# Kernel optimization log

Hardware: AMD Instinct MI355X
Metric: run time of the kernel (lower is better)

Reference implementation:

```python
import jax, jax.numpy as jnp
import numpy as np

NUM_EXPERTS = 8
TOP_K = 2
ENTROPY_WEIGHT = 0.1
MAX_USAGE_RATIO = 0.3


def setup_inputs() -> dict:
    key = jax.random.key(0)
    k0, k1, k2 = jax.random.split(key, 3)
    B, S, D, H, E = 4, 4096, 1024, 1024, NUM_EXPERTS
    x = jax.random.normal(k0, (B, S, D), jnp.float32)
    gate_w = jax.random.normal(k1, (D, E), jnp.float32) * (1.0 / np.sqrt(D))
    gate_b = jnp.zeros((E,), jnp.float32)
    expert_w = jax.random.normal(k2, (E, D, H), jnp.float32) * (1.0 / np.sqrt(D))
    expert_b = jnp.zeros((E, H), jnp.float32)
    return {"x": x, "gate_w": gate_w, "gate_b": gate_b,
            "expert_w": expert_w, "expert_b": expert_b}


def reference(x, gate_w, gate_b, expert_w, expert_b):
    # x: [B, S, D]; dropout omitted (eval mode / deterministic reference)
    B, S, D = x.shape
    E = gate_w.shape[1]
    H = expert_w.shape[2]
    N = B * S
    xf = x.reshape(N, D)

    gate_logits = xf @ gate_w + gate_b            # [N, E]
    gate_probs = jax.nn.softmax(gate_logits, axis=-1)
    entropy = -jnp.sum(gate_probs * jnp.log(gate_probs + 1e-10), axis=-1).mean()
    entropy_loss = ENTROPY_WEIGHT * entropy

    topk_probs, topk_idx = jax.lax.top_k(gate_probs, TOP_K)   # [N, K]
    onehot = jax.nn.one_hot(topk_idx, E, dtype=xf.dtype)       # [N, K, E]
    combine = jnp.einsum('nk,nke->ne', topk_probs, onehot)     # [N, E] gating weight per expert

    # Weighted combine of per-expert Linear outputs; loop over small fixed E.
    out = jnp.zeros((N, H), xf.dtype)
    for e in range(E):
        out = out + combine[:, e:e + 1] * (xf @ expert_w[e] + expert_b[e])

    counts = jnp.sum(onehot, axis=(0, 1))                      # [E] tokens routed per expert
    usage_ratios = counts / N
    overuse_penalty = jnp.sum(jax.nn.relu(usage_ratios - MAX_USAGE_RATIO))

    return out.reshape(B, S, H), entropy_loss + overuse_penalty
```

## Files before the change

### kernel.cpp

```cpp
#include <hip/hip_runtime.h>
#include <hip/hip_bf16.h>

typedef __bf16 bf16x8 __attribute__((ext_vector_type(8)));
typedef __bf16 bf16x4 __attribute__((ext_vector_type(4)));
typedef float  f32x4  __attribute__((ext_vector_type(4)));

#define NTOK 16384
#define DDIM 1024
#define HDIM 1024
#define NEXP 8

#define XB_OFF   0u
#define WT_OFF   33554432u
#define IDX_OFF  50331648u
#define PRB_OFF  50855936u
#define TTE_OFF  51380224u
#define TTP_OFF  51511296u
#define CNT_OFF  51642368u
#define ENT_OFF  51642400u

typedef __attribute__((address_space(1))) void gvoid_t;
typedef __attribute__((address_space(3))) void lvoid_t;

__device__ __forceinline__ void cp16(void* lds, const void* g) {
  __builtin_amdgcn_global_load_lds((gvoid_t*)g, (lvoid_t*)lds, 16, 0, 0);
}

__global__ __launch_bounds__(256) void transpose_w(const float* __restrict__ w,
                                                   __bf16* __restrict__ wT) {
  const int e  = blockIdx.z;
  const int d0 = blockIdx.y * 64;
  const int h0 = blockIdx.x * 64;
  __shared__ float tile[64][68];
  const int t = threadIdx.x;
  const float* base = w + ((size_t)e * DDIM + d0) * HDIM + h0;
#pragma unroll
  for (int it = 0; it < 4; ++it) {
    int dl = it * 16 + (t >> 4);
    int hl = (t & 15) * 4;
    float4 v = *(const float4*)(base + (size_t)dl * HDIM + hl);
    tile[dl][hl]     = v.x;
    tile[dl][hl + 1] = v.y;
    tile[dl][hl + 2] = v.z;
    tile[dl][hl + 3] = v.w;
  }
  __syncthreads();
  __bf16* obase = wT + ((size_t)e * HDIM + h0) * DDIM + d0;
#pragma unroll
  for (int it = 0; it < 4; ++it) {
    int hl = it * 16 + (t >> 4);
    int dl = (t & 15) * 4;
    bf16x4 bv;
    bv[0] = (__bf16)tile[dl][hl];
    bv[1] = (__bf16)tile[dl + 1][hl];
    bv[2] = (__bf16)tile[dl + 2][hl];
    bv[3] = (__bf16)tile[dl + 3][hl];
    *(bf16x4*)(obase + (size_t)hl * DDIM + dl) = bv;
  }
}

__global__ __launch_bounds__(256) void gate_kernel(
    const float* __restrict__ x, const float* __restrict__ gw,
    const float* __restrict__ gb, __bf16* __restrict__ xb,
    int* __restrict__ idx_g, float* __restrict__ prob_g,
    int2* __restrict__ tt_e, float2* __restrict__ tt_p,
    int* __restrict__ cnt_g, float* __restrict__ ent_g) {
  __shared__ float gwT[8 * 1040];
  __shared__ int   lidx[8 * 64];
  __shared__ float lprob[8 * 64];
  __shared__ int   lcnt[8];
  __shared__ int   gbase[8];
  __shared__ float went[4];
  const int tid = threadIdx.x, w = tid >> 6, lane = tid & 63;
  if (tid < 8) lcnt[tid] = 0;
#pragma unroll
  for (int i = 0; i < 32; ++i) {
    int lin = i * 256 + tid;
    gwT[(lin & 7) * 1040 + (lin >> 3)] = gw[lin];
  }
  __syncthreads();

  float entacc = 0.f;
  for (int t = 0; t < 8; ++t) {
    const int n = blockIdx.x * 32 + w * 8 + t;
    const float4* xr = (const float4*)(x + (size_t)n * DDIM);
    float acc[8] = {0.f, 0.f, 0.f, 0.f, 0.f, 0.f, 0.f, 0.f};
#pragma unroll
    for (int i = 0; i < 4; ++i) {
      float4 v = xr[i * 64 + lane];
      bf16x4 bv;
      bv[0] = (__bf16)v.x; bv[1] = (__bf16)v.y;
      bv[2] = (__bf16)v.z; bv[3] = (__bf16)v.w;
      *(bf16x4*)(xb + (size_t)n * DDIM + i * 256 + lane * 4) = bv;
#pragma unroll
      for (int e = 0; e < 8; ++e) {
        float4 g = *(const float4*)&gwT[e * 1040 + i * 256 + lane * 4];
        acc[e] += v.x * g.x + v.y * g.y + v.z * g.z + v.w * g.w;
      }
    }
#pragma unroll
    for (int e = 0; e < 8; ++e) {
      float s = acc[e];
      for (int off = 32; off; off >>= 1) s += __shfl_down(s, off);
      acc[e] = s;
    }
    if (lane == 0) {
      float p[8];
      float mx = -1e30f;
#pragma unroll
      for (int e = 0; e < 8; ++e) { p[e] = acc[e] + gb[e]; mx = fmaxf(mx, p[e]); }
      float s = 0.f;
#pragma unroll
      for (int e = 0; e < 8; ++e) { p[e] = expf(p[e] - mx); s += p[e]; }
      float inv = 1.0f / s;
      float ent = 0.f;
#pragma unroll
      for (int e = 0; e < 8; ++e) { p[e] *= inv; ent -= p[e] * logf(p[e] + 1e-10f); }
      entacc += ent;
      int e1 = 0; float p1 = p[0];
#pragma unroll
      for (int e = 1; e < 8; ++e) if (p[e] > p1) { p1 = p[e]; e1 = e; }
      int e2 = (e1 == 0) ? 1 : 0; float p2 = p[e2];
#pragma unroll
      for (int e = 0; e < 8; ++e) if (e != e1 && p[e] > p2) { p2 = p[e]; e2 = e; }
      tt_e[n] = make_int2(e1, e2);
      tt_p[n] = make_float2(p1, p2);
      int j = atomicAdd(&lcnt[e1], 1); lidx[e1 * 64 + j] = n; lprob[e1 * 64 + j] = p1;
      j = atomicAdd(&lcnt[e2], 1);     lidx[e2 * 64 + j] = n; lprob[e2 * 64 + j] = p2;
    }
  }
  if (lane == 0) went[w] = entacc;
  __syncthreads();
  if (tid < 8) gbase[tid] = atomicAdd(&cnt_g[tid], lcnt[tid]);
  if (tid == 0) atomicAdd(ent_g, went[0] + went[1] + went[2] + went[3]);
  __syncthreads();
#pragma unroll
  for (int e = 0; e < 8; ++e) {
    for (int j = tid; j < lcnt[e]; j += 256) {
      idx_g[e * NTOK + gbase[e] + j]  = lidx[e * 64 + j];
      prob_g[e * NTOK + gbase[e] + j] = lprob[e * 64 + j];
    }
  }
}

__global__ __launch_bounds__(256) void init_out(const int2* __restrict__ tt_e,
                                                const float2* __restrict__ tt_p,
                                                const float* __restrict__ eb,
                                                float* __restrict__ out) {
  const int n = blockIdx.x, t = threadIdx.x;
  int2   ee = tt_e[n];
  float2 pp = tt_p[n];
  float4 v1 = ((const float4*)(eb + (size_t)ee.x * HDIM))[t];
  float4 v2 = ((const float4*)(eb + (size_t)ee.y * HDIM))[t];
  float4 r;
  r.x = pp.x * v1.x + pp.y * v2.x;
  r.y = pp.x * v1.y + pp.y * v2.y;
  r.z = pp.x * v1.z + pp.y * v2.z;
  r.w = pp.x * v1.w + pp.y * v2.w;
  ((float4*)(out + (size_t)n * HDIM))[t] = r;
}

__global__ __launch_bounds__(256) void moe_gemm(
    const __bf16* __restrict__ xb, const __bf16* __restrict__ wT,
    const int* __restrict__ idx_g, const float* __restrict__ prob_g,
    const int* __restrict__ cnt_g, float* __restrict__ out) {
  const int e = blockIdx.z, gy = blockIdx.y, gx = blockIdx.x;
  const int cnt = cnt_g[e];
  if (gy * 128 >= cnt) return;

  __shared__ __bf16 Ash[128 * 64];
  __shared__ __bf16 Bsh[128 * 64];
  __shared__ int    tok_s[128];
  __shared__ float  p_s[128];

  const int tid = threadIdx.x, w = tid >> 6, lane = tid & 63;
  if (tid < 128) {
    int gm  = gy * 128 + tid;
    int src = (gm < cnt) ? gm : (cnt - 1);
    tok_s[tid] = idx_g[e * NTOK + src];
    p_s[tid]   = (gm < cnt) ? prob_g[e * NTOK + src] : 0.0f;
  }
  __syncthreads();

  f32x4 acc[4][4];
  const f32x4 zero = {0.f, 0.f, 0.f, 0.f};
#pragma unroll
  for (int mi = 0; mi < 4; ++mi)
#pragma unroll
    for (int ni = 0; ni < 4; ++ni) acc[mi][ni] = zero;

  const __bf16* wbase = wT + (size_t)e * HDIM * DDIM + (size_t)(gx * 128) * DDIM;
  const int wm = (w >> 1) * 64, wn = (w & 1) * 64;
  const int tq = lane >> 4, tr = lane & 15;
  const int rsub = lane >> 3, c = lane & 7;

  for (int kk = 0; kk < 16; ++kk) {
    const int k0 = kk * 64;
#pragma unroll
    for (int it = 0; it < 4; ++it) {
      int rb = it * 32 + w * 8;
      int r  = rb + rsub;
      cp16((char*)Ash + rb * 128,
           xb + (size_t)tok_s[r] * DDIM + k0 + c * 8);
    }
#pragma unroll
    for (int it = 0; it < 4; ++it) {
      int rb = it * 32 + w * 8;
      int r  = rb + rsub;
      cp16((char*)Bsh + rb * 128,
           wbase + (size_t)r * DDIM + k0 + c * 8);
    }
    __syncthreads();
#pragma unroll
    for (int h = 0; h < 2; ++h) {
      bf16x8 a[4], b[4];
#pragma unroll
      for (int mi = 0; mi < 4; ++mi)
        a[mi] = *(const bf16x8*)((const char*)Ash + (wm + mi * 16 + tr) * 128 + h * 64 + tq * 16);
#pragma unroll
      for (int ni = 0; ni < 4; ++ni)
        b[ni] = *(const bf16x8*)((const char*)Bsh + (wn + ni * 16 + tr) * 128 + h * 64 + tq * 16);
#pragma unroll
      for (int mi = 0; mi < 4; ++mi)
#pragma unroll
        for (int ni = 0; ni < 4; ++ni)
          acc[mi][ni] = __builtin_amdgcn_mfma_f32_16x16x32_bf16(a[mi], b[ni], acc[mi][ni], 0, 0, 0);
    }
    __syncthreads();
  }

#pragma unroll
  for (int mi = 0; mi < 4; ++mi) {
#pragma unroll
    for (int r = 0; r < 4; ++r) {
      int lr = wm + mi * 16 + tq * 4 + r;
      int gm = gy * 128 + lr;
      if (gm < cnt) {
        int   tok = tok_s[lr];
        float p   = p_s[lr];
        float* orow = out + (size_t)tok * HDIM + gx * 128 + wn + tr;
#pragma unroll
        for (int ni = 0; ni < 4; ++ni)
          atomicAdd(orow + ni * 16, p * acc[mi][ni][r]);
      }
    }
  }
}

__global__ void finalize(const float* __restrict__ ent_g, const int* __restrict__ cnt_g,
                         float* __restrict__ loss_out) {
  if (threadIdx.x == 0) {
    float ent = ent_g[0] / (float)NTOK;
    float pen = 0.f;
    for (int e = 0; e < 8; ++e) {
      float r = (float)cnt_g[e] / (float)NTOK - 0.3f;
      if (r > 0.f) pen += r;
    }
    loss_out[0] = 0.1f * ent + pen;
  }
}

extern "C" void kernel_launch(void* const* d_in, const int* in_sizes, int n_in,
                              void* d_out, int out_size, void* d_ws, size_t ws_size,
                              hipStream_t stream) {
  const float* x  = (const float*)d_in[0];
  const float* gw = (const float*)d_in[1];
  const float* gb = (const float*)d_in[2];
  const float* ew = (const float*)d_in[3];
  const float* eb = (const float*)d_in[4];
  float* out = (float*)d_out;
  char*  ws  = (char*)d_ws;

  __bf16* xb     = (__bf16*)(ws + XB_OFF);
  __bf16* wT     = (__bf16*)(ws + WT_OFF);
  int*    idx_g  = (int*)(ws + IDX_OFF);
  float*  prob_g = (float*)(ws + PRB_OFF);
  int2*   tt_e   = (int2*)(ws + TTE_OFF);
  float2* tt_p   = (float2*)(ws + TTP_OFF);
  int*    cnt_g  = (int*)(ws + CNT_OFF);
  float*  ent_g  = (float*)(ws + ENT_OFF);

  hipMemsetAsync(ws + CNT_OFF, 0, 64, stream);
  transpose_w<<<dim3(16, 16, 8), 256, 0, stream>>>(ew, wT);
  gate_kernel<<<dim3(NTOK / 32), 256, 0, stream>>>(x, gw, gb, xb, idx_g, prob_g,
                                                   tt_e, tt_p, cnt_g, ent_g);
  init_out<<<dim3(NTOK), 256, 0, stream>>>(tt_e, tt_p, eb, out);
  moe_gemm<<<dim3(8, 128, 8), 256, 0, stream>>>(xb, wT, idx_g, prob_g, cnt_g, out);
  finalize<<<1, 64, 0, stream>>>(ent_g, cnt_g, out + (size_t)NTOK * HDIM);
}
```

Before: 344.1 us.

## Fuse weight transpose, gating and output init into one prep kernel; swizzle GEMM LDS

Merges the weight transpose, gating and bias-init kernels into a single prep launch whose blocks split by index between the transpose and gating roles. The output bias init now happens inside gating, which removes the intermediate top-k buffers and one launch. The GEMM's LDS layout gets an XOR swizzle to cut bank conflicts on MFMA operand reads. Expert counters are padded onto separate cache lines to reduce atomic contention, and gating now runs 16 tokens per block with all lanes doing softmax via xor-shuffles.

Result: slower. 362.1 us (+5.2%).

```diff
diff --git a/kernel.cpp b/kernel.cpp
--- a/kernel.cpp
+++ b/kernel.cpp
@@ -9,15 +9,14 @@
 #define DDIM 1024
 #define HDIM 1024
 #define NEXP 8
+#define CNT_STRIDE 16
 
 #define XB_OFF   0u
 #define WT_OFF   33554432u
 #define IDX_OFF  50331648u
 #define PRB_OFF  50855936u
-#define TTE_OFF  51380224u
-#define TTP_OFF  51511296u
-#define CNT_OFF  51642368u
-#define ENT_OFF  51642400u
+#define CNT_OFF  51380224u
+#define ENT_OFF  51380736u
 
 typedef __attribute__((address_space(1))) void gvoid_t;
 typedef __attribute__((address_space(3))) void lvoid_t;
@@ -26,138 +25,148 @@
   __builtin_amdgcn_global_load_lds((gvoid_t*)g, (lvoid_t*)lds, 16, 0, 0);
 }
 
-__global__ __launch_bounds__(256) void transpose_w(const float* __restrict__ w,
-                                                   __bf16* __restrict__ wT) {
-  const int e  = blockIdx.z;
-  const int d0 = blockIdx.y * 64;
-  const int h0 = blockIdx.x * 64;
-  __shared__ float tile[64][68];
-  const int t = threadIdx.x;
-  const float* base = w + ((size_t)e * DDIM + d0) * HDIM + h0;
-#pragma unroll
-  for (int it = 0; it < 4; ++it) {
-    int dl = it * 16 + (t >> 4);
-    int hl = (t & 15) * 4;
-    float4 v = *(const float4*)(base + (size_t)dl * HDIM + hl);
-    tile[dl][hl]     = v.x;
-    tile[dl][hl + 1] = v.y;
-    tile[dl][hl + 2] = v.z;
-    tile[dl][hl + 3] = v.w;
-  }
-  __syncthreads();
-  __bf16* obase = wT + ((size_t)e * HDIM + h0) * DDIM + d0;
-#pragma unroll
-  for (int it = 0; it < 4; ++it) {
-    int hl = it * 16 + (t >> 4);
-    int dl = (t & 15) * 4;
-    bf16x4 bv;
-    bv[0] = (__bf16)tile[dl][hl];
-    bv[1] = (__bf16)tile[dl + 1][hl];
-    bv[2] = (__bf16)tile[dl + 2][hl];
-    bv[3] = (__bf16)tile[dl + 3][hl];
-    *(bf16x4*)(obase + (size_t)hl * DDIM + dl) = bv;
-  }
-}
-
-__global__ __launch_bounds__(256) void gate_kernel(
+union SmemU {
+  float tile[64][68];
+  struct {
+    float gwT[8 * 1032];
+    int   lidx[8 * 32];
+    float lprob[8 * 32];
+    int   lcnt[8];
+    int   gbase[8];
+    float went[4];
+  } g;
+};
+
+__global__ __launch_bounds__(256) void prep_kernel(
     const float* __restrict__ x, const float* __restrict__ gw,
-    const float* __restrict__ gb, __bf16* __restrict__ xb,
-    int* __restrict__ idx_g, float* __restrict__ prob_g,
-    int2* __restrict__ tt_e, float2* __restrict__ tt_p,
-    int* __restrict__ cnt_g, float* __restrict__ ent_g) {
-  __shared__ float gwT[8 * 1040];
-  __shared__ int   lidx[8 * 64];
-  __shared__ float lprob[8 * 64];
-  __shared__ int   lcnt[8];
-  __shared__ int   gbase[8];
-  __shared__ float went[4];
-  const int tid = threadIdx.x, w = tid >> 6, lane = tid & 63;
-  if (tid < 8) lcnt[tid] = 0;
+    const float* __restrict__ gb, const float* __restrict__ ew,
+    const float* __restrict__ eb, __bf16* __restrict__ xb,
+    __bf16* __restrict__ wT, int* __restrict__ idx_g,
+    float* __restrict__ prob_g, int* __restrict__ cnt_g,
+    float* __restrict__ ent_g, float* __restrict__ out) {
+  __shared__ SmemU sm;
+  const int tid = threadIdx.x;
+
+  if (blockIdx.x < 2048) {
+    const int b  = blockIdx.x;
+    const int e  = b >> 8;
+    const int d0 = ((b >> 4) & 15) * 64;
+    const int h0 = (b & 15) * 64;
+    const float* base = ew + ((size_t)e * DDIM + d0) * HDIM + h0;
+#pragma unroll
+    for (int it = 0; it < 4; ++it) {
+      int dl = it * 16 + (tid >> 4);
+      int hl = (tid & 15) * 4;
+      float4 v = *(const float4*)(base + (size_t)dl * HDIM + hl);
+      sm.tile[dl][hl]     = v.x;
+      sm.tile[dl][hl + 1] = v.y;
+      sm.tile[dl][hl + 2] = v.z;
+      sm.tile[dl][hl + 3] = v.w;
+    }
+    __syncthreads();
+    __bf16* obase = wT + ((size_t)e * HDIM + h0) * DDIM + d0;
+#pragma unroll
+    for (int it = 0; it < 4; ++it) {
+      int hl = it * 16 + (tid >> 4);
+      int dl = (tid & 15) * 4;
+      bf16x4 bv;
+      bv[0] = (__bf16)sm.tile[dl][hl];
+      bv[1] = (__bf16)sm.tile[dl + 1][hl];
+      bv[2] = (__bf16)sm.tile[dl + 2][hl];
+      bv[3] = (__bf16)sm.tile[dl + 3][hl];
+      *(bf16x4*)(obase + (size_t)hl * DDIM + dl) = bv;
+    }
+    return;
+  }
+
+  const int gbid = blockIdx.x - 2048;
+  const int w = tid >> 6, lane = tid & 63;
+  if (tid < 8) sm.g.lcnt[tid] = 0;
 #pragma unroll
   for (int i = 0; i < 32; ++i) {
     int lin = i * 256 + tid;
-    gwT[(lin & 7) * 1040 + (lin >> 3)] = gw[lin];
-  }
+    sm.g.gwT[(lin & 7) * 1032 + (lin >> 3)] = gw[lin];
+  }
+  float gbr[8];
+#pragma unroll
+  for (int e = 0; e < 8; ++e) gbr[e] = gb[e];
   __syncthreads();
 
   float entacc = 0.f;
-  for (int t = 0; t < 8; ++t) {
-    const int n = blockIdx.x * 32 + w * 8 + t;
-    const float4* xr = (const float4*)(x + (size_t)n * DDIM);
+  for (int t = 0; t < 4; ++t) {
+    const int n = gbid * 16 + w * 4 + t;
     float acc[8] = {0.f, 0.f, 0.f, 0.f, 0.f, 0.f, 0.f, 0.f};
 #pragma unroll
-    for (int i = 0; i < 4; ++i) {
-      float4 v = xr[i * 64 + lane];
+    for (int j = 0; j < 4; ++j) {
+      float4 v = *(const float4*)(x + (size_t)n * DDIM + j * 256 + lane * 4);
       bf16x4 bv;
       bv[0] = (__bf16)v.x; bv[1] = (__bf16)v.y;
       bv[2] = (__bf16)v.z; bv[3] = (__bf16)v.w;
-      *(bf16x4*)(xb + (size_t)n * DDIM + i * 256 + lane * 4) = bv;
+      *(bf16x4*)(xb + (size_t)n * DDIM + j * 256 + lane * 4) = bv;
 #pragma unroll
       for (int e = 0; e < 8; ++e) {
-        float4 g = *(const float4*)&gwT[e * 1040 + i * 256 + lane * 4];
+        float4 g = *(const float4*)&sm.g.gwT[e * 1032 + j * 256 + lane * 4];
         acc[e] += v.x * g.x + v.y * g.y + v.z * g.z + v.w * g.w;
       }
     }
 #pragma unroll
     for (int e = 0; e < 8; ++e) {
       float s = acc[e];
-      for (int off = 32; off; off >>= 1) s += __shfl_down(s, off);
+#pragma unroll
+      for (int off = 1; off < 64; off <<= 1) s += __shfl_xor(s, off);
       acc[e] = s;
     }
+    float p[8];
+    float mx = -1e30f;
+#pragma unroll
+    for (int e = 0; e < 8; ++e) { p[e] = acc[e] + gbr[e]; mx = fmaxf(mx, p[e]); }
+    float s = 0.f;
+#pragma unroll
+    for (int e = 0; e < 8; ++e) { p[e] = expf(p[e] - mx); s += p[e]; }
+    float inv = 1.0f / s;
+    float ent = 0.f;
+#pragma unroll
+    for (int e = 0; e < 8; ++e) { p[e] *= inv; ent -= p[e] * logf(p[e] + 1e-10f); }
+    entacc += ent;
+    int e1 = 0; float p1 = p[0];
+#pragma unroll
+    for (int e = 1; e < 8; ++e) if (p[e] > p1) { p1 = p[e]; e1 = e; }
+    int e2 = (e1 == 0) ? 1 : 0; float p2 = p[e2];
+#pragma unroll
+    for (int e = 0; e < 8; ++e) if (e != e1 && p[e] > p2) { p2 = p[e]; e2 = e; }
     if (lane == 0) {
-      float p[8];
-      float mx = -1e30f;
-#pragma unroll
-      for (int e = 0; e < 8; ++e) { p[e] = acc[e] + gb[e]; mx = fmaxf(mx, p[e]); }
-      float s = 0.f;
-#pragma unroll
-      for (int e = 0; e < 8; ++e) { p[e] = expf(p[e] - mx); s += p[e]; }
-      float inv = 1.0f / s;
-      float ent = 0.f;
-#pragma unroll
-      for (int e = 0; e < 8; ++e) { p[e] *= inv; ent -= p[e] * logf(p[e] + 1e-10f); }
-      entacc += ent;
-      int e1 = 0; float p1 = p[0];
-#pragma unroll
-      for (int e = 1; e < 8; ++e) if (p[e] > p1) { p1 = p[e]; e1 = e; }
-      int e2 = (e1 == 0) ? 1 : 0; float p2 = p[e2];
-#pragma unroll
-      for (int e = 0; e < 8; ++e) if (e != e1 && p[e] > p2) { p2 = p[e]; e2 = e; }
-      tt_e[n] = make_int2(e1, e2);
-      tt_p[n] = make_float2(p1, p2);
-      int j = atomicAdd(&lcnt[e1], 1); lidx[e1 * 64 + j] = n; lprob[e1 * 64 + j] = p1;
-      j = atomicAdd(&lcnt[e2], 1);     lidx[e2 * 64 + j] = n; lprob[e2 * 64 + j] = p2;
-    }
-  }
-  if (lane == 0) went[w] = entacc;
+      int j = atomicAdd(&sm.g.lcnt[e1], 1);
+      sm.g.lidx[e1 * 32 + j] = n; sm.g.lprob[e1 * 32 + j] = p1;
+      j = atomicAdd(&sm.g.lcnt[e2], 1);
+      sm.g.lidx[e2 * 32 + j] = n; sm.g.lprob[e2 * 32 + j] = p2;
+    }
+    const float4* b1 = (const float4*)(eb + (size_t)e1 * HDIM);
+    const float4* b2 = (const float4*)(eb + (size_t)e2 * HDIM);
+    float4* orow = (float4*)(out + (size_t)n * HDIM);
+#pragma unroll
+    for (int j = 0; j < 4; ++j) {
+      int hi = j * 64 + lane;
+      float4 v1 = b1[hi], v2 = b2[hi], r;
+      r.x = p1 * v1.x + p2 * v2.x;
+      r.y = p1 * v1.y + p2 * v2.y;
+      r.z = p1 * v1.z + p2 * v2.z;
+      r.w = p1 * v1.w + p2 * v2.w;
+      orow[hi] = r;
+    }
+  }
+  if (lane == 0) sm.g.went[w] = entacc;
   __syncthreads();
-  if (tid < 8) gbase[tid] = atomicAdd(&cnt_g[tid], lcnt[tid]);
-  if (tid == 0) atomicAdd(ent_g, went[0] + went[1] + went[2] + went[3]);
+  if (tid < 8) sm.g.gbase[tid] = atomicAdd(&cnt_g[tid * CNT_STRIDE], sm.g.lcnt[tid]);
+  if (tid == 0)
+    atomicAdd(ent_g, sm.g.went[0] + sm.g.went[1] + sm.g.went[2] + sm.g.went[3]);
   __syncthreads();
 #pragma unroll
   for (int e = 0; e < 8; ++e) {
-    for (int j = tid; j < lcnt[e]; j += 256) {
-      idx_g[e * NTOK + gbase[e] + j]  = lidx[e * 64 + j];
-      prob_g[e * NTOK + gbase[e] + j] = lprob[e * 64 + j];
-    }
-  }
-}
-
-__global__ __launch_bounds__(256) void init_out(const int2* __restrict__ tt_e,
-                                                const float2* __restrict__ tt_p,
-                                                const float* __restrict__ eb,
-                                                float* __restrict__ out) {
-  const int n = blockIdx.x, t = threadIdx.x;
-  int2   ee = tt_e[n];
-  float2 pp = tt_p[n];
-  float4 v1 = ((const float4*)(eb + (size_t)ee.x * HDIM))[t];
-  float4 v2 = ((const float4*)(eb + (size_t)ee.y * HDIM))[t];
-  float4 r;
-  r.x = pp.x * v1.x + pp.y * v2.x;
-  r.y = pp.x * v1.y + pp.y * v2.y;
-  r.z = pp.x * v1.z + pp.y * v2.z;
-  r.w = pp.x * v1.w + pp.y * v2.w;
-  ((float4*)(out + (size_t)n * HDIM))[t] = r;
+    for (int j = tid; j < sm.g.lcnt[e]; j += 256) {
+      idx_g[e * NTOK + sm.g.gbase[e] + j]  = sm.g.lidx[e * 32 + j];
+      prob_g[e * NTOK + sm.g.gbase[e] + j] = sm.g.lprob[e * 32 + j];
+    }
+  }
 }
 
 __global__ __launch_bounds__(256) void moe_gemm(
@@ -165,8 +174,8 @@
     const int* __restrict__ idx_g, const float* __restrict__ prob_g,
     const int* __restrict__ cnt_g, float* __restrict__ out) {
   const int e = blockIdx.z, gy = blockIdx.y, gx = blockIdx.x;
-  const int cnt = cnt_g[e];
-  if (gy * 128 >= cnt) return;
+  const int cnt = cnt_g[e * CNT_STRIDE];
+  if (cnt == 0 || gy * 128 >= cnt) return;
 
   __shared__ __bf16 Ash[128 * 64];
   __shared__ __bf16 Bsh[128 * 64];
@@ -191,8 +200,9 @@
 
   const __bf16* wbase = wT + (size_t)e * HDIM * DDIM + (size_t)(gx * 128) * DDIM;
   const int wm = (w >> 1) * 64, wn = (w & 1) * 64;
-  const int tq = lane >> 4, tr = lane & 15;
-  const int rsub = lane >> 3, c = lane & 7;
+  const int tq = lane >> 4, tr = lane & 15, tr7 = tr & 7;
+  const int rsub = lane >> 3;
+  const int csw = ((lane & 7) ^ (rsub & 7)) * 8;
 
   for (int kk = 0; kk < 16; ++kk) {
     const int k0 = kk * 64;
@@ -201,25 +211,31 @@
       int rb = it * 32 + w * 8;
       int r  = rb + rsub;
       cp16((char*)Ash + rb * 128,
-           xb + (size_t)tok_s[r] * DDIM + k0 + c * 8);
+           xb + (size_t)tok_s[r] * DDIM + k0 + csw);
     }
 #pragma unroll
     for (int it = 0; it < 4; ++it) {
       int rb = it * 32 + w * 8;
       int r  = rb + rsub;
       cp16((char*)Bsh + rb * 128,
-           wbase + (size_t)r * DDIM + k0 + c * 8);
+           wbase + (size_t)r * DDIM + k0 + csw);
     }
     __syncthreads();
 #pragma unroll
     for (int h = 0; h < 2; ++h) {
       bf16x8 a[4], b[4];
 #pragma unroll
-      for (int mi = 0; mi < 4; ++mi)
-        a[mi] = *(const bf16x8*)((const char*)Ash + (wm + mi * 16 + tr) * 128 + h * 64 + tq * 16);
-#pragma unroll
-      for (int ni = 0; ni < 4; ++ni)
-        b[ni] = *(const bf16x8*)((const char*)Bsh + (wn + ni * 16 + tr) * 128 + h * 64 + tq * 16);
+      for (int mi = 0; mi < 4; ++mi) {
+        int row = wm + mi * 16 + tr;
+        a[mi] = *(const bf16x8*)((const char*)Ash + row * 128 +
+                                 ((((h << 2) | tq) ^ tr7) << 4));
+      }
+#pragma unroll
+      for (int ni = 0; ni < 4; ++ni) {
+        int row = wn + ni * 16 + tr;
+        b[ni] = *(const bf16x8*)((const char*)Bsh + row * 128 +
+                                 ((((h << 2) | tq) ^ tr7) << 4));
+      }
 #pragma unroll
       for (int mi = 0; mi < 4; ++mi)
 #pragma unroll
@@ -253,7 +269,7 @@
     float ent = ent_g[0] / (float)NTOK;
     float pen = 0.f;
     for (int e = 0; e < 8; ++e) {
-      float r = (float)cnt_g[e] / (float)NTOK - 0.3f;
+      float r = (float)cnt_g[e * CNT_STRIDE] / (float)NTOK - 0.3f;
       if (r > 0.f) pen += r;
     }
     loss_out[0] = 0.1f * ent + pen;
@@ -275,16 +291,12 @@
   __bf16* wT     = (__bf16*)(ws + WT_OFF);
   int*    idx_g  = (int*)(ws + IDX_OFF);
   float*  prob_g = (float*)(ws + PRB_OFF);
-  int2*   tt_e   = (int2*)(ws + TTE_OFF);
-  float2* tt_p   = (float2*)(ws + TTP_OFF);
   int*    cnt_g  = (int*)(ws + CNT_OFF);
   float*  ent_g  = (float*)(ws + ENT_OFF);
 
-  hipMemsetAsync(ws + CNT_OFF, 0, 64, stream);
-  transpose_w<<<dim3(16, 16, 8), 256, 0, stream>>>(ew, wT);
-  gate_kernel<<<dim3(NTOK / 32), 256, 0, stream>>>(x, gw, gb, xb, idx_g, prob_g,
-                                                   tt_e, tt_p, cnt_g, ent_g);
-  init_out<<<dim3(NTOK), 256, 0, stream>>>(tt_e, tt_p, eb, out);
+  hipMemsetAsync(ws + CNT_OFF, 0, 1024, stream);
+  prep_kernel<<<dim3(3072), 256, 0, stream>>>(x, gw, gb, ew, eb, xb, wT,
+                                              idx_g, prob_g, cnt_g, ent_g, out);
   moe_gemm<<<dim3(8, 128, 8), 256, 0, stream>>>(xb, wT, idx_g, prob_g, cnt_g, out);
   finalize<<<1, 64, 0, stream>>>(ent_g, cnt_g, out + (size_t)NTOK * HDIM);
 }
```
